# Kernel optimization log

Measured on AMD Instinct MI355X. Metric: run time of the kernel, lower is better.

The kernel has to match this reference:

```python
import jax, jax.numpy as jnp
import numpy as np

B, N, P, E = 64, 512, 256, 4096          # batch, nodes (stations), partition nodes, edges
NUM_NWP, LP, F = 8, 16, 32               # num_nwp, local_points, local_cnn_dims
NT, ED, H, W = 8, 8, 64, 8               # num_temp, edge_feature_dims, decf_mlp_hidden, weight_function_dim
G, RH = 64, 256                          # gnn_dim, readout_hid_dim
H1, Q = 128, 9                           # mlp_hid_dim1, num quantiles


def setup_inputs() -> dict:
    key = jax.random.key(0)
    ks = iter(jax.random.split(key, 40))
    def rn(shape, s=0.05):
        return jax.random.normal(next(ks), shape, dtype=jnp.float32) * s
    # one-hot incidence matrices: each edge has one left (partition) node and one right node
    lidx = jax.random.randint(next(ks), (E,), 0, P)
    ridx = jax.random.randint(next(ks), (E,), 0, N)
    linc = jnp.zeros((P, E), jnp.float32).at[lidx, jnp.arange(E)].set(1.0)
    rinc = jnp.zeros((E, N), jnp.float32).at[jnp.arange(E), ridx].set(1.0)
    inp = {
        "x1": jax.random.normal(next(ks), (B, NUM_NWP * N, LP), dtype=jnp.float32),
        "x2": jax.random.normal(next(ks), (B, NT), dtype=jnp.float32),
        # LocalConv1D grouped conv (torch OIW layout: [Cout, Cin/groups, K])
        "conv_w": rn((F * N, NUM_NWP, LP)), "conv_b": rn((F * N,)),
        # WDSGCN2 edge-weight MLP
        "k1_w": rn((H, ED)), "k1_b": rn((H,)),
        "k2_w": rn((H, NT)),
        "k3_w": rn((H, F)),
        "k4_w": rn((H, F)),
        "k5_w": rn((W, H)), "k5_b": rn((W,)),
        "gc_w": rn((G, F * W)), "gc_b": rn((G,)),
        # readout
        "r0_w": rn((RH, G * P)),
        "r1_w": rn((RH, NT)), "r1_b": rn((RH,)),
        "r2_w": rn((RH, P)),
        "r3_w": rn((P, RH)), "r3_b": rn((P,)),
        # SMlp (forward uses l1 -> ELU -> l3 only)
        "l1_w": rn((H1, NT + G)), "l1_b": rn((H1,)),
        "l3_w": rn((Q, H1)), "l3_b": rn((Q,)),
        # buffers
        "ef": jax.random.normal(next(ks), (E, ED + 1), dtype=jnp.float32),
        "linc": linc,
        "rinc": rinc,
        "cap_feature": jax.random.normal(next(ks), (P,), dtype=jnp.float32),
        "partition_idx": jnp.arange(P, dtype=jnp.int32) * (N // P),
    }
    return inp


def reference(x1, x2, conv_w, conv_b, k1_w, k1_b, k2_w, k3_w, k4_w, k5_w, k5_b,
              gc_w, gc_b, r0_w, r1_w, r1_b, r2_w, r3_w, r3_b,
              l1_w, l1_b, l3_w, l3_b, ef, linc, rinc, cap_feature, partition_idx):
    b = x1.shape[0]
    # --- LocalConv1D: grouped conv1d (valid padding, output length 1) + ReLU ---
    y = jax.lax.conv_general_dilated(x1, conv_w, (1,), 'VALID',
                                     dimension_numbers=('NCH', 'OIH', 'NCH'),
                                     feature_group_count=N)
    x = jax.nn.relu(y + conv_b[None, :, None]).reshape(b, N, F)      # [B,N,F]
    # --- WDSGCN2: per-edge weight kernel ---
    kern = ef[:, :-1] @ k1_w.T + k1_b                                # [E,H]
    kern = kern[None] + (x2 @ k2_w.T)[:, None, :]                    # [B,E,H]
    xp = x[:, partition_idx, :]                                      # [B,P,F]
    kern = kern + jnp.einsum('pe,bpf->bef', linc, xp) @ k3_w.T       # left-node feats
    rx = jnp.einsum('en,bnf->bef', rinc, x)                          # right-node feats [B,E,F]
    kern = kern + rx @ k4_w.T
    kern = jax.nn.relu(jax.nn.leaky_relu(kern, 0.02) @ k5_w.T + k5_b)  # [B,E,W]
    # --- message = kernel (outer) right-node features, aggregated by left incidence ---
    msg = kern[:, :, :, None] * rx[:, :, None, :]                    # [B,E,W,F]
    agg = jnp.einsum('pe,bewf->bpwf', linc, msg).reshape(b, P, W * F)
    yg = jax.nn.relu(agg @ gc_w.T + gc_b)                            # [B,P,G]
    # --- readout attention over partition nodes ---
    h = yg.reshape(b, -1) @ r0_w.T + (x2 @ r1_w.T + r1_b) + cap_feature @ r2_w.T
    wt = jax.nn.relu(jax.nn.leaky_relu(h, 0.01) @ r3_w.T + r3_b)     # [B,P]
    res = jnp.einsum('bp,bpg->bg', wt, yg)                           # [B,G]
    # --- SMlp head ---
    z = jnp.concatenate([res, x2], axis=1)
    z = jax.nn.elu(z @ l1_w.T + l1_b)
    return z @ l3_w.T + l3_b                                         # [B,Q]
```

## Files before the change

kernel.cpp:

```cpp
#include <hip/hip_runtime.h>
#include <math.h>

#define B_ 64
#define N_ 512
#define P_ 256
#define E_ 4096
#define F_ 32
#define H_ 64
#define W_ 8
#define G_ 64
#define RH_ 256

#define X_OFF   0
#define T4_OFF  (X_OFF + N_*B_*F_)
#define T3_OFF  (T4_OFF + N_*B_*H_)
#define KB_OFF  (T3_OFF + P_*B_*H_)
#define KW_OFF  (KB_OFF + E_*H_)
#define YG_OFF  (KW_OFF + E_*B_*W_)
#define HB_OFF  (YG_OFF + B_*P_*G_)
#define RES_OFF (HB_OFF + B_*RH_)
#define INT_OFF (RES_OFF + 4*B_*G_)
#define PART_OFF (INT_OFF + 20480)

__global__ __launch_bounds__(256) void k_dc(const float* __restrict__ linc,
    const float* __restrict__ rinc, int* __restrict__ lidx, int* __restrict__ ridx,
    const float* __restrict__ x1, const float* __restrict__ conv_w,
    const float* __restrict__ conv_b, float* __restrict__ x) {
  __shared__ float wsm[32 * 132];
  __shared__ float xsm[8192];
  int blk = blockIdx.x, t = threadIdx.x;
  if (blk < 3072) {
    int i4 = blk * 256 + t;
    const int L4 = (P_ * E_) / 4;
    if (i4 < L4) {
      float4 v = ((const float4*)linc)[i4];
      int i = i4 * 4;
      int p = i >> 12, e = i & 4095;
      if (v.x != 0.0f) lidx[e]     = p;
      if (v.y != 0.0f) lidx[e + 1] = p;
      if (v.z != 0.0f) lidx[e + 2] = p;
      if (v.w != 0.0f) lidx[e + 3] = p;
    } else {
      int j4 = i4 - L4;
      float4 v = ((const float4*)rinc)[j4];
      int j = j4 * 4;
      int e = j >> 9, n = j & 511;
      if (v.x != 0.0f) ridx[e] = n;
      if (v.y != 0.0f) ridx[e] = n + 1;
      if (v.z != 0.0f) ridx[e] = n + 2;
      if (v.w != 0.0f) ridx[e] = n + 3;
    }
    return;
  }
  int n = blk - 3072;
  for (int i = t; i < 1024; i += 256) {
    int f = i >> 5, j = i & 31;
    ((float4*)wsm)[f * 33 + j] = ((const float4*)(conv_w + n * 4096))[i];
  }
  for (int i = t; i < 2048; i += 256) {
    int b = i >> 5, j = i & 31;
    ((float4*)xsm)[i] = ((const float4*)(x1 + b * 65536 + n * 128))[j];
  }
  __syncthreads();
  int f = t & 31, bq = t >> 5;
  float cb = conv_b[n * 32 + f];
  float acc[8];
#pragma unroll
  for (int bi = 0; bi < 8; bi++) acc[bi] = cb;
  const float4* wf4 = (const float4*)wsm + f * 33;
  const float4* xb4 = (const float4*)xsm + bq * 256;
#pragma unroll 4
  for (int k4 = 0; k4 < 32; k4++) {
    float4 wv = wf4[k4];
#pragma unroll
    for (int bi = 0; bi < 8; bi++) {
      float4 xv = xb4[bi * 32 + k4];
      acc[bi] += wv.x * xv.x + wv.y * xv.y + wv.z * xv.z + wv.w * xv.w;
    }
  }
#pragma unroll
  for (int bi = 0; bi < 8; bi++) {
    int b = bq * 8 + bi;
    x[n * 2048 + b * 32 + f] = fmaxf(acc[bi], 0.0f);
  }
}

__global__ __launch_bounds__(1024) void k_lists(const int* __restrict__ lidx,
    const int* __restrict__ ridx, int* __restrict__ part_start,
    int* __restrict__ part_edges, int* __restrict__ r_s) {
  __shared__ int cnt[256];
  __shared__ int buf[256];
  __shared__ int cur[256];
  int t = threadIdx.x;
  if (t < 256) cnt[t] = 0;
  __syncthreads();
  for (int e = t; e < E_; e += 1024) atomicAdd(&cnt[lidx[e]], 1);
  __syncthreads();
  if (t < 256) buf[t] = cnt[t];
  __syncthreads();
  for (int off = 1; off < 256; off <<= 1) {
    int add = 0;
    if (t < 256 && t >= off) add = buf[t - off];
    __syncthreads();
    if (t < 256) buf[t] += add;
    __syncthreads();
  }
  if (t < 256) {
    part_start[t + 1] = buf[t];
    if (t == 0) part_start[0] = 0;
    cur[t] = buf[t] - cnt[t];
  }
  __syncthreads();
  for (int e = t; e < E_; e += 1024) {
    int p = lidx[e];
    int pos = atomicAdd(&cur[p], 1);
    part_edges[pos] = e;
  }
  __syncthreads();
  for (int pos = t; pos < E_; pos += 1024) r_s[pos] = ridx[part_edges[pos]];
}

__global__ __launch_bounds__(256) void k_prep(
    const float* __restrict__ x, const int* __restrict__ pidx,
    const float* __restrict__ k3_w, const float* __restrict__ k4_w,
    const float* __restrict__ x2, const float* __restrict__ k2_w,
    const float* __restrict__ ef, const float* __restrict__ k1_w,
    const float* __restrict__ k1_b,
    const float* __restrict__ r1_w, const float* __restrict__ r1_b,
    const float* __restrict__ r2_w, const float* __restrict__ cap,
    float* __restrict__ t4, float* __restrict__ t3, float* __restrict__ kb,
    float* __restrict__ hbuf) {
  __shared__ float xsh[2048];
  __shared__ float wsh[64 * 36];
  __shared__ float x2s[512];
  __shared__ float k2s[512];
  int blk = blockIdx.x, t = threadIdx.x;
  if (blk < 768) {
    bool isT4 = blk < 512;
    int n = isT4 ? blk : pidx[blk - 512];
    const float* wmat = isT4 ? k4_w : k3_w;
    float* outp = isT4 ? (t4 + blk * 4096) : (t3 + (blk - 512) * 4096);
    for (int i = t; i < 512; i += 256) {
      ((float4*)xsh)[i] = ((const float4*)(x + n * 2048))[i];
      int h = i >> 3, j = i & 7;
      ((float4*)wsh)[h * 9 + j] = ((const float4*)wmat)[i];
    }
    if (isT4) {
      for (int i = t; i < 128; i += 256) {
        ((float4*)x2s)[i] = ((const float4*)x2)[i];
        ((float4*)k2s)[i] = ((const float4*)k2_w)[i];
      }
    }
    __syncthreads();
    int h = t & 63, bq = t >> 6;
    float wreg[32];
#pragma unroll
    for (int j = 0; j < 8; j++) {
      float4 v = ((float4*)wsh)[h * 9 + j];
      wreg[4 * j] = v.x; wreg[4 * j + 1] = v.y; wreg[4 * j + 2] = v.z; wreg[4 * j + 3] = v.w;
    }
    float w2[8];
    if (isT4) {
      float4 u = ((float4*)k2s)[h * 2], v = ((float4*)k2s)[h * 2 + 1];
      w2[0] = u.x; w2[1] = u.y; w2[2] = u.z; w2[3] = u.w;
      w2[4] = v.x; w2[5] = v.y; w2[6] = v.z; w2[7] = v.w;
    }
    for (int bi = 0; bi < 16; bi++) {
      int b = bq * 16 + bi;
      float acc = 0.0f;
#pragma unroll
      for (int j = 0; j < 8; j++) {
        float4 xv = ((float4*)xsh)[b * 8 + j];
        acc += xv.x * wreg[4 * j] + xv.y * wreg[4 * j + 1] +
               xv.z * wreg[4 * j + 2] + xv.w * wreg[4 * j + 3];
      }
      if (isT4) {
        float4 u = ((float4*)x2s)[b * 2], v = ((float4*)x2s)[b * 2 + 1];
        acc += u.x * w2[0] + u.y * w2[1] + u.z * w2[2] + u.w * w2[3] +
               v.x * w2[4] + v.y * w2[5] + v.z * w2[6] + v.w * w2[7];
      }
      outp[b * 64 + h] = acc;
    }
  } else if (blk < 1792) {
    int o = (blk - 768) * 256 + t;
    int e = o >> 6, h = o & 63;
    float acc = k1_b[h];
    const float* er = ef + e * 9;
    const float* kr = k1_w + h * 8;
#pragma unroll
    for (int d = 0; d < 8; d++) acc += er[d] * kr[d];
    kb[o] = acc;
  } else {
    int o = (blk - 1792) * 256 + t;
    int rh = o & 255;
    float acc = r1_b[rh];
    const float* xr = x2 + (o >> 8) * 8;
    const float* rr = r1_w + rh * 8;
#pragma unroll
    for (int d = 0; d < 8; d++) acc += xr[d] * rr[d];
    const float* r2r = r2_w + rh * 256;
    for (int p4 = 0; p4 < 64; p4++) {
      float4 cv = ((const float4*)cap)[p4];
      float4 rv = ((const float4*)r2r)[p4];
      acc += cv.x * rv.x + cv.y * rv.y + cv.z * rv.z + cv.w * rv.w;
    }
    hbuf[o] = acc;
  }
}

__global__ __launch_bounds__(256) void k_edge(
    const float* __restrict__ kb, const float* __restrict__ t3,
    const float* __restrict__ t4, const float* __restrict__ k5_w,
    const float* __restrict__ k5_b, const int* __restrict__ lidx,
    const int* __restrict__ ridx, const int* __restrict__ part_edges,
    float* __restrict__ kw_s) {
  __shared__ float k5t[4 * 520];
  int pos0 = blockIdx.x * 4, t = threadIdx.x;
  for (int i = t; i < 512; i += 256) {
    int h = i >> 3, w = i & 7;
    float v = k5_w[w * 64 + h];
#pragma unroll
    for (int qq = 0; qq < 4; qq++) k5t[qq * 520 + i] = v;
  }
  int q = t & 3, b = t >> 2;
  const float* kq = k5t + q * 520 + q * 128;
  float kb5_0 = k5_b[2 * q], kb5_1 = k5_b[2 * q + 1];
  __syncthreads();
  for (int ei = 0; ei < 4; ei++) {
    int pos = pos0 + ei;
    int e = part_edges[pos];
    int p = lidx[e], r = ridx[e];
    const float4* kb4 = (const float4*)(kb + e * 64 + q * 16);
    const float4* t34 = (const float4*)(t3 + p * 4096 + b * 64 + q * 16);
    const float4* t44 = (const float4*)(t4 + r * 4096 + b * 64 + q * 16);
    float lk[16];
#pragma unroll
    for (int j4 = 0; j4 < 4; j4++) {
      float4 a = kb4[j4], c = t34[j4], d = t44[j4];
      float v;
      v = a.x + c.x + d.x; lk[j4 * 4 + 0] = v > 0.0f ? v : 0.02f * v;
      v = a.y + c.y + d.y; lk[j4 * 4 + 1] = v > 0.0f ? v : 0.02f * v;
      v = a.z + c.z + d.z; lk[j4 * 4 + 2] = v > 0.0f ? v : 0.02f * v;
      v = a.w + c.w + d.w; lk[j4 * 4 + 3] = v > 0.0f ? v : 0.02f * v;
    }
    float pw[8] = {0, 0, 0, 0, 0, 0, 0, 0};
#pragma unroll
    for (int j = 0; j < 16; j++) {
      float4 u = *(const float4*)(kq + j * 8);
      float4 v = *(const float4*)(kq + j * 8 + 4);
      float l = lk[j];
      pw[0] += l * u.x; pw[1] += l * u.y; pw[2] += l * u.z; pw[3] += l * u.w;
      pw[4] += l * v.x; pw[5] += l * v.y; pw[6] += l * v.z; pw[7] += l * v.w;
    }
#pragma unroll
    for (int w = 0; w < 8; w++) {
      pw[w] += __shfl_xor(pw[w], 1);
      pw[w] += __shfl_xor(pw[w], 2);
    }
    float2 o;
    o.x = fmaxf(pw[2 * q] + kb5_0, 0.0f);
    o.y = fmaxf(pw[2 * q + 1] + kb5_1, 0.0f);
    *(float2*)(kw_s + pos * 512 + t * 2) = o;
  }
}

__global__ __launch_bounds__(256) void k_agg(
    const float* __restrict__ x, const float* __restrict__ kw_s,
    const int* __restrict__ r_s, const int* __restrict__ part_start,
    const float* __restrict__ gc_w, const float* __restrict__ gc_b,
    float* __restrict__ yg) {
  __shared__ float accS[32 * 256];
  int blk = blockIdx.x, t = threadIdx.x;
  int p = blk & 255, bsub = blk >> 8;
  int bl = t >> 3, fs = t & 7;
  int b = bsub * 32 + bl;
  float acc[8][4];
#pragma unroll
  for (int w = 0; w < 8; w++)
#pragma unroll
    for (int j = 0; j < 4; j++) acc[w][j] = 0.0f;
  int s0 = part_start[p], s1 = part_start[p + 1];
  const float* xb = x + b * 32 + fs * 4;
  const float* kwb = kw_s + b * 8;
  int r_cur = 0;
  float4 ka_cur = make_float4(0, 0, 0, 0), kc_cur = make_float4(0, 0, 0, 0);
  if (s0 < s1) {
    r_cur = r_s[s0];
    const float4* kp = (const float4*)(kwb + (size_t)s0 * 512);
    ka_cur = kp[0]; kc_cur = kp[1];
  }
  for (int pos = s0; pos < s1; pos++) {
    int r_n = r_cur;
    float4 ka_n = ka_cur, kc_n = kc_cur;
    if (pos + 1 < s1) {
      r_n = r_s[pos + 1];
      const float4* kp = (const float4*)(kwb + (size_t)(pos + 1) * 512);
      ka_n = kp[0]; kc_n = kp[1];
    }
    float4 xv = *(const float4*)(xb + r_cur * 2048);
    float kw[8] = {ka_cur.x, ka_cur.y, ka_cur.z, ka_cur.w,
                   kc_cur.x, kc_cur.y, kc_cur.z, kc_cur.w};
#pragma unroll
    for (int w = 0; w < 8; w++) {
      acc[w][0] += kw[w] * xv.x;
      acc[w][1] += kw[w] * xv.y;
      acc[w][2] += kw[w] * xv.z;
      acc[w][3] += kw[w] * xv.w;
    }
    r_cur = r_n; ka_cur = ka_n; kc_cur = kc_n;
  }
  int swz = (bl >> 2) & 7;
#pragma unroll
  for (int w = 0; w < 8; w++) {
    int oct = w * 4 + (fs >> 1);
    int po = oct ^ swz;
    float* dst = accS + bl * 256 + po * 8 + (fs & 1) * 4;
    *(float4*)dst = make_float4(acc[w][0], acc[w][1], acc[w][2], acc[w][3]);
  }
  __syncthreads();
  int lane = t & 63, wv = t >> 6;
  int q = lane >> 3, gg = lane & 7;
  int g0 = wv * 16 + gg * 2;
  const float* gw0 = gc_w + g0 * 256;
  const float* gw1 = gw0 + 256;
  float ac[4][2];
#pragma unroll
  for (int i = 0; i < 4; i++) { ac[i][0] = 0.0f; ac[i][1] = 0.0f; }
  for (int oct = 0; oct < 32; oct++) {
    int po = oct ^ q;
    float4 b0a = *(const float4*)(gw0 + oct * 8);
    float4 b0b = *(const float4*)(gw0 + oct * 8 + 4);
    float4 b1a = *(const float4*)(gw1 + oct * 8);
    float4 b1b = *(const float4*)(gw1 + oct * 8 + 4);
    float bv0[8] = {b0a.x, b0a.y, b0a.z, b0a.w, b0b.x, b0b.y, b0b.z, b0b.w};
    float bv1[8] = {b1a.x, b1a.y, b1a.z, b1a.w, b1b.x, b1b.y, b1b.z, b1b.w};
#pragma unroll
    for (int i = 0; i < 4; i++) {
      const float* sp = accS + (4 * q + i) * 256 + po * 8;
      float4 aa = *(const float4*)sp;
      float4 ab = *(const float4*)(sp + 4);
      float av[8] = {aa.x, aa.y, aa.z, aa.w, ab.x, ab.y, ab.z, ab.w};
#pragma unroll
      for (int kk = 0; kk < 8; kk++) {
        ac[i][0] += av[kk] * bv0[kk];
        ac[i][1] += av[kk] * bv1[kk];
      }
    }
  }
  float gb0 = gc_b[g0], gb1 = gc_b[g0 + 1];
#pragma unroll
  for (int i = 0; i < 4; i++) {
    int bo = bsub * 32 + 4 * q + i;
    float2 o;
    o.x = fmaxf(ac[i][0] + gb0, 0.0f);
    o.y = fmaxf(ac[i][1] + gb1, 0.0f);
    *(float2*)(yg + bo * 16384 + p * 64 + g0) = o;
  }
}

__global__ __launch_bounds__(256) void k_r0(const float* __restrict__ yg,
    const float* __restrict__ r0_w, float* __restrict__ part) {
  __shared__ float ygs[32 * 69];
  __shared__ float wts[32 * 260];
  int kc = blockIdx.x, t = threadIdx.x;
  int k0 = kc * 32;
  {
    int c = t >> 5, rr = t & 31;
    for (int rd = 0; rd < 8; rd++) {
      int rh = rd * 32 + rr;
      float4 v = *(const float4*)(r0_w + rh * 16384 + k0 + c * 4);
      wts[(4 * c + 0) * 260 + rh] = v.x;
      wts[(4 * c + 1) * 260 + rh] = v.y;
      wts[(4 * c + 2) * 260 + rh] = v.z;
      wts[(4 * c + 3) * 260 + rh] = v.w;
    }
  }
  {
    int b = t >> 2, kq = t & 3;
    const float* src = yg + b * 16384 + k0 + kq * 8;
#pragma unroll
    for (int uu = 0; uu < 2; uu++) {
      float4 v = *(const float4*)(src + uu * 4);
      int kk = kq * 8 + uu * 4;
      ygs[(kk + 0) * 69 + b] = v.x;
      ygs[(kk + 1) * 69 + b] = v.y;
      ygs[(kk + 2) * 69 + b] = v.z;
      ygs[(kk + 3) * 69 + b] = v.w;
    }
  }
  __syncthreads();
  int lane = t & 63, wv = t >> 6;
  int b8 = lane & 7, r8 = lane >> 3;
  const float* yp = ygs + b8 * 8;
  const float* wp = wts + wv * 64 + r8 * 8;
  float acc[8][8];
#pragma unroll
  for (int i = 0; i < 8; i++)
#pragma unroll
    for (int j = 0; j < 8; j++) acc[i][j] = 0.0f;
#pragma unroll 2
  for (int k = 0; k < 32; k++) {
    float4 ya = *(const float4*)(yp + k * 69);
    float4 yb = *(const float4*)(yp + k * 69 + 4);
    float4 wa = *(const float4*)(wp + k * 260);
    float4 wb = *(const float4*)(wp + k * 260 + 4);
    float yv[8] = {ya.x, ya.y, ya.z, ya.w, yb.x, yb.y, yb.z, yb.w};
    float wr[8] = {wa.x, wa.y, wa.z, wa.w, wb.x, wb.y, wb.z, wb.w};
#pragma unroll
    for (int i = 0; i < 8; i++)
#pragma unroll
      for (int j = 0; j < 8; j++) acc[i][j] += yv[i] * wr[j];
  }
  float* pb = part + kc * 16384 + wv * 64 + r8 * 8;
#pragma unroll
  for (int i = 0; i < 8; i++) {
    float4 s0 = make_float4(acc[i][0], acc[i][1], acc[i][2], acc[i][3]);
    float4 s1 = make_float4(acc[i][4], acc[i][5], acc[i][6], acc[i][7]);
    float* pp = pb + (b8 * 8 + i) * 256;
    *(float4*)pp = s0;
    *(float4*)(pp + 4) = s1;
  }
}

__global__ __launch_bounds__(256) void k_r0red(const float* __restrict__ part,
    float* __restrict__ hbuf) {
  int blk = blockIdx.x;
  int oq = blk & 63, kq = blk >> 6;
  int o = oq * 256 + threadIdx.x;
  float s = 0.0f;
  const float* pp = part + kq * 64 * 16384 + o;
#pragma unroll 8
  for (int kc = 0; kc < 64; kc++) s += pp[kc * 16384];
  atomicAdd(&hbuf[o], s);
}

__global__ __launch_bounds__(256) void k_wt_res(const float* __restrict__ hbuf,
    const float* __restrict__ r3_w, const float* __restrict__ r3_b,
    const float* __restrict__ yg, float* __restrict__ res4) {
  __shared__ float hs[256];
  __shared__ float wts[64];
  __shared__ float red[256];
  int blk = blockIdx.x;
  int bb = blk >> 2, pq = blk & 3;
  int t = threadIdx.x;
  float hv = hbuf[bb * 256 + t];
  hs[t] = hv > 0.0f ? hv : 0.01f * hv;
  __syncthreads();
  int pl = t >> 2, c = t & 3;
  int pp = pq * 64 + pl;
  const float4* wrow = (const float4*)(r3_w + pp * 256 + c * 64);
  const float4* h4 = (const float4*)(hs) + c * 16;
  float a = 0.0f;
#pragma unroll
  for (int j = 0; j < 16; j++) {
    float4 w4 = wrow[j], hh = h4[j];
    a += hh.x * w4.x + hh.y * w4.y + hh.z * w4.z + hh.w * w4.w;
  }
  a += __shfl_xor(a, 1);
  a += __shfl_xor(a, 2);
  if (c == 0) wts[pl] = fmaxf(a + r3_b[pp], 0.0f);
  __syncthreads();
  int g = t & 63, ch = t >> 6;
  float r = 0.0f;
  const float* ygp = yg + bb * 16384 + pq * 4096 + g;
#pragma unroll
  for (int pi = 0; pi < 16; pi++) {
    int pl2 = ch * 16 + pi;
    r += wts[pl2] * ygp[pl2 * 64];
  }
  red[t] = r;
  __syncthreads();
  if (t < 64)
    res4[pq * 4096 + bb * 64 + t] = red[t] + red[t + 64] + red[t + 128] + red[t + 192];
}

__global__ __launch_bounds__(128) void k_final(const float* __restrict__ res4,
    const float* __restrict__ x2, const float* __restrict__ l1_w,
    const float* __restrict__ l1_b, const float* __restrict__ l3_w,
    const float* __restrict__ l3_b, float* __restrict__ out) {
  __shared__ float zs[128];
  int bb = blockIdx.x, t = threadIdx.x;
  float acc = l1_b[t];
  const float* wrow = l1_w + t * 72;
  const float* rr = res4 + bb * 64;
#pragma unroll 8
  for (int j = 0; j < 64; j++) {
    float rv = rr[j] + rr[4096 + j] + rr[8192 + j] + rr[12288 + j];
    acc += rv * wrow[j];
  }
  const float* xr = x2 + bb * 8;
#pragma unroll
  for (int j = 0; j < 8; j++) acc += xr[j] * wrow[64 + j];
  zs[t] = acc > 0.0f ? acc : expm1f(acc);
  __syncthreads();
  if (t < 9) {
    float o = l3_b[t];
    const float* w3 = l3_w + t * 128;
    for (int j = 0; j < 128; j++) o += zs[j] * w3[j];
    out[bb * 9 + t] = o;
  }
}

extern "C" void kernel_launch(void* const* d_in, const int* in_sizes, int n_in,
                              void* d_out, int out_size, void* d_ws, size_t ws_size,
                              hipStream_t stream) {
  (void)in_sizes; (void)n_in; (void)out_size; (void)ws_size;
  const float* x1     = (const float*)d_in[0];
  const float* x2     = (const float*)d_in[1];
  const float* conv_w = (const float*)d_in[2];
  const float* conv_b = (const float*)d_in[3];
  const float* k1_w   = (const float*)d_in[4];
  const float* k1_b   = (const float*)d_in[5];
  const float* k2_w   = (const float*)d_in[6];
  const float* k3_w   = (const float*)d_in[7];
  const float* k4_w   = (const float*)d_in[8];
  const float* k5_w   = (const float*)d_in[9];
  const float* k5_b   = (const float*)d_in[10];
  const float* gc_w   = (const float*)d_in[11];
  const float* gc_b   = (const float*)d_in[12];
  const float* r0_w   = (const float*)d_in[13];
  const float* r1_w   = (const float*)d_in[14];
  const float* r1_b   = (const float*)d_in[15];
  const float* r2_w   = (const float*)d_in[16];
  const float* r3_w   = (const float*)d_in[17];
  const float* r3_b   = (const float*)d_in[18];
  const float* l1_w   = (const float*)d_in[19];
  const float* l1_b   = (const float*)d_in[20];
  const float* l3_w   = (const float*)d_in[21];
  const float* l3_b   = (const float*)d_in[22];
  const float* ef     = (const float*)d_in[23];
  const float* linc   = (const float*)d_in[24];
  const float* rinc   = (const float*)d_in[25];
  const float* cap    = (const float*)d_in[26];
  const int*   pidx   = (const int*)d_in[27];
  float* out = (float*)d_out;

  float* ws   = (float*)d_ws;
  float* xbuf = ws + X_OFF;
  float* t4   = ws + T4_OFF;
  float* t3   = ws + T3_OFF;
  float* kb   = ws + KB_OFF;
  float* kw_s = ws + KW_OFF;
  float* yg   = ws + YG_OFF;
  float* hbuf = ws + HB_OFF;
  float* res4 = ws + RES_OFF;
  float* part = ws + PART_OFF;
  int* ib = (int*)(ws + INT_OFF);
  int* lidx = ib;
  int* ridx = ib + 4096;
  int* part_start = ib + 8192;
  int* part_edges = ib + 8704;
  int* r_s = ib + 12800;

  hipLaunchKernelGGL(k_dc, dim3(3584), dim3(256), 0, stream,
                     linc, rinc, lidx, ridx, x1, conv_w, conv_b, xbuf);
  hipLaunchKernelGGL(k_lists, dim3(1), dim3(1024), 0, stream,
                     lidx, ridx, part_start, part_edges, r_s);
  hipLaunchKernelGGL(k_prep, dim3(1856), dim3(256), 0, stream,
                     xbuf, pidx, k3_w, k4_w, x2, k2_w, ef, k1_w, k1_b,
                     r1_w, r1_b, r2_w, cap, t4, t3, kb, hbuf);
  hipLaunchKernelGGL(k_edge, dim3(1024), dim3(256), 0, stream,
                     kb, t3, t4, k5_w, k5_b, lidx, ridx, part_edges, kw_s);
  hipLaunchKernelGGL(k_agg, dim3(512), dim3(256), 0, stream,
                     xbuf, kw_s, r_s, part_start, gc_w, gc_b, yg);
  hipLaunchKernelGGL(k_r0, dim3(512), dim3(256), 0, stream, yg, r0_w, part);
  hipLaunchKernelGGL(k_r0red, dim3(512), dim3(256), 0, stream, part, hbuf);
  hipLaunchKernelGGL(k_wt_res, dim3(256), dim3(256), 0, stream, hbuf, r3_w, r3_b, yg, res4);
  hipLaunchKernelGGL(k_final, dim3(64), dim3(128), 0, stream,
                     res4, x2, l1_w, l1_b, l3_w, l3_b, out);
}
```

Measured before the change: 277.5 us.

## Stage gathered x rows and edge kernels through shared memory in k_agg

The aggregation loop used to do a per-thread serial gather, where each thread loaded its own float4 of x and its kernel weights for each edge, with a one-step software prefetch. Now the block cooperatively loads 8 edges at once, one edge per 32-thread group, reading contiguous rows of x and kw. It writes them into padded shared memory tiles, then all threads accumulate from shared memory. This aims for wider, coalesced global loads and more memory-level parallelism, at the cost of extra shared memory (about 44KB total, which may lower occupancy) and two barriers per 8-edge chunk.

```diff
diff --git a/kernel.cpp b/kernel.cpp
--- a/kernel.cpp
+++ b/kernel.cpp
@@ -269,46 +269,64 @@
     const int* __restrict__ r_s, const int* __restrict__ part_start,
     const float* __restrict__ gc_w, const float* __restrict__ gc_b,
     float* __restrict__ yg) {
+  __shared__ float xS[8 * 1152];
+  __shared__ float kwS[8 * 256];
   __shared__ float accS[32 * 256];
   int blk = blockIdx.x, t = threadIdx.x;
   int p = blk & 255, bsub = blk >> 8;
   int bl = t >> 3, fs = t & 7;
-  int b = bsub * 32 + bl;
   float acc[8][4];
 #pragma unroll
   for (int w = 0; w < 8; w++)
 #pragma unroll
     for (int j = 0; j < 4; j++) acc[w][j] = 0.0f;
   int s0 = part_start[p], s1 = part_start[p + 1];
-  const float* xb = x + b * 32 + fs * 4;
-  const float* kwb = kw_s + b * 8;
-  int r_cur = 0;
-  float4 ka_cur = make_float4(0, 0, 0, 0), kc_cur = make_float4(0, 0, 0, 0);
-  if (s0 < s1) {
-    r_cur = r_s[s0];
-    const float4* kp = (const float4*)(kwb + (size_t)s0 * 512);
-    ka_cur = kp[0]; kc_cur = kp[1];
-  }
-  for (int pos = s0; pos < s1; pos++) {
-    int r_n = r_cur;
-    float4 ka_n = ka_cur, kc_n = kc_cur;
-    if (pos + 1 < s1) {
-      r_n = r_s[pos + 1];
-      const float4* kp = (const float4*)(kwb + (size_t)(pos + 1) * 512);
-      ka_n = kp[0]; kc_n = kp[1];
-    }
-    float4 xv = *(const float4*)(xb + r_cur * 2048);
-    float kw[8] = {ka_cur.x, ka_cur.y, ka_cur.z, ka_cur.w,
-                   kc_cur.x, kc_cur.y, kc_cur.z, kc_cur.w};
-#pragma unroll
-    for (int w = 0; w < 8; w++) {
-      acc[w][0] += kw[w] * xv.x;
-      acc[w][1] += kw[w] * xv.y;
-      acc[w][2] += kw[w] * xv.z;
-      acc[w][3] += kw[w] * xv.w;
-    }
-    r_cur = r_n; ka_cur = ka_n; kc_cur = kc_n;
-  }
+  int se = t >> 5;
+  int sl = t & 31;
+  for (int base = s0; base < s1; base += 8) {
+    int pos = base + se;
+    int posc = (pos < s1) ? pos : (s1 - 1);
+    int r = r_s[posc];
+    const float4* xsrc = (const float4*)(x + (size_t)r * 2048 + bsub * 1024);
+    float4 xr[8];
+#pragma unroll
+    for (int k = 0; k < 8; k++) xr[k] = xsrc[sl + k * 32];
+    const float4* ksrc = (const float4*)(kw_s + (size_t)posc * 512 + bsub * 256);
+    float4 kw0 = ksrc[sl];
+    float4 kw1 = ksrc[sl + 32];
+    __syncthreads();
+    float* xrow = xS + se * 1152;
+#pragma unroll
+    for (int k = 0; k < 8; k++) {
+      int m = sl + k * 32;
+      int b = m >> 3, fq = m & 7;
+      *(float4*)(xrow + b * 36 + fq * 4) = xr[k];
+    }
+    {
+      float* krow = kwS + se * 256;
+      int b0 = sl >> 1, h0 = sl & 1;
+      *(float4*)(krow + b0 * 8 + h0 * 4) = kw0;
+      int m1 = sl + 32;
+      int b1 = m1 >> 1, h1 = m1 & 1;
+      *(float4*)(krow + b1 * 8 + h1 * 4) = kw1;
+    }
+    __syncthreads();
+    int lim = s1 - base; if (lim > 8) lim = 8;
+    for (int i = 0; i < lim; i++) {
+      float4 xv = *(const float4*)(xS + i * 1152 + bl * 36 + fs * 4);
+      float4 ka = *(const float4*)(kwS + i * 256 + bl * 8);
+      float4 kc = *(const float4*)(kwS + i * 256 + bl * 8 + 4);
+      float kw[8] = {ka.x, ka.y, ka.z, ka.w, kc.x, kc.y, kc.z, kc.w};
+#pragma unroll
+      for (int w = 0; w < 8; w++) {
+        acc[w][0] += kw[w] * xv.x;
+        acc[w][1] += kw[w] * xv.y;
+        acc[w][2] += kw[w] * xv.z;
+        acc[w][3] += kw[w] * xv.w;
+      }
+    }
+  }
+  __syncthreads();
   int swz = (bl >> 2) & 7;
 #pragma unroll
   for (int w = 0; w < 8; w++) {
```

After: 290.8 us. 4.8% more time.
